# Performance work log

Hardware: AMD Instinct MI355X
Metric: run time of the kernel (lower is better)

Reference implementation:

```python
import jax, jax.numpy as jnp
import numpy as np

DIM = 512
HEADS = 8
RES = 14
HEAD_DIM = DIM // HEADS
N = RES * RES


def _make_bias_idxs(res):
    pts = [(i, j) for i in range(res) for j in range(res)]
    offs = {}
    idxs = []
    for p1 in pts:
        for p2 in pts:
            o = (abs(p1[0] - p2[0]), abs(p1[1] - p2[1]))
            if o not in offs:
                offs[o] = len(offs)
            idxs.append(offs[o])
    return np.asarray(idxs, dtype=np.int32).reshape(res * res, res * res), len(offs)


def setup_inputs() -> dict:
    key = jax.random.key(0)
    ks = jax.random.split(key, 6)
    idxs, n_off = _make_bias_idxs(RES)  # n_off == 196 for res=14
    B = 128
    return {
        "x": jax.random.normal(ks[0], (B, DIM, RES, RES), dtype=jnp.float32),
        "qkv_w": jax.random.normal(ks[1], (3 * DIM, DIM), dtype=jnp.float32) * 0.02,
        "qkv_b": jnp.zeros((3 * DIM,), dtype=jnp.float32),
        "proj_w": jax.random.normal(ks[2], (DIM, DIM), dtype=jnp.float32) * 0.02,
        "proj_b": jnp.zeros((DIM,), dtype=jnp.float32),
        "attention_biases": jax.random.normal(ks[3], (HEADS, n_off), dtype=jnp.float32) * 0.02,
        "bias_idxs": jnp.asarray(idxs),
    }


def reference(x, qkv_w, qkv_b, proj_w, proj_b, attention_biases, bias_idxs):
    B, C, H, W = x.shape
    scale = HEAD_DIM ** -0.5
    # 1x1 conv == channel-wise linear
    qkv = jnp.einsum("oc,bchw->bohw", qkv_w, x) + qkv_b[None, :, None, None]
    q, k, v = jnp.split(qkv, 3, axis=1)
    # [B, heads, head_dim, N]
    q = q.reshape(B, HEADS, HEAD_DIM, N)
    k = k.reshape(B, HEADS, HEAD_DIM, N)
    v = v.reshape(B, HEADS, HEAD_DIM, N)
    attn = jnp.einsum("bhdn,bhdm->bhnm", q, k) * scale  # [B,h,N,N]
    bias = attention_biases[:, bias_idxs]  # gather -> [h,N,N]
    attn = jax.nn.softmax(attn + bias[None], axis=-1)
    out = jnp.einsum("bhnm,bhdm->bhdn", attn, v).reshape(B, C, H, W)
    return jnp.einsum("oc,bchw->bohw", proj_w, out) + proj_b[None, :, None, None]
```

## Files before the change

kernel.cpp:

```cpp
#include <hip/hip_runtime.h>
#include <hip/hip_bf16.h>
#include <math.h>

#define B_     128
#define DIM_   512
#define HEADS_ 8
#define HD_    64
#define N_     196
#define NP_    224
#define NROW_  208
#define SCALE_ 0.125f
#define BSTRIDE (DIM_ * N_)
#define J_     (B_ * NP_)

typedef unsigned short u16;
typedef unsigned int   u32;
typedef __attribute__((ext_vector_type(8))) short bf16x8;
typedef __attribute__((ext_vector_type(4))) float f32x4;

__device__ __forceinline__ u16 f2bf(float f) {
    u32 u = __float_as_uint(f);
    return (u16)((u + 0x7fffu + ((u >> 16) & 1u)) >> 16);
}


__global__ __launch_bounds__(256) void cvt_w2(
    const float* __restrict__ qw, u16* __restrict__ qd,
    const float* __restrict__ pw, u16* __restrict__ pd)
{
    const float* src = blockIdx.y ? pw : qw;
    u16* dst = blockIdx.y ? pd : qd;
    const int nch = blockIdx.y ? (DIM_ * DIM_ / 8) : (3 * DIM_ * DIM_ / 8);
    const int t = blockIdx.x * 256 + threadIdx.x;
    if (t < nch) {
        const int m16 = t & 15, q = (t >> 4) & 3, kb = (t >> 6) & 15, mb = t >> 10;
        const float* s = src + (size_t)(mb * 16 + m16) * DIM_ + kb * 32 + q * 8;
        const float4 v0 = reinterpret_cast<const float4*>(s)[0];
        const float4 v1 = reinterpret_cast<const float4*>(s)[1];
        uint4 o;
        o.x = (u32)f2bf(v0.x) | ((u32)f2bf(v0.y) << 16);
        o.y = (u32)f2bf(v0.z) | ((u32)f2bf(v0.w) << 16);
        o.z = (u32)f2bf(v1.x) | ((u32)f2bf(v1.y) << 16);
        o.w = (u32)f2bf(v1.z) | ((u32)f2bf(v1.w) << 16);
        reinterpret_cast<uint4*>(dst)[t] = o;
    }
}

__global__ __launch_bounds__(256) void cvt_xT(
    const float* __restrict__ x, u16* __restrict__ XT)
{
    __shared__ float tile[64][65];
    const int t = threadIdx.x;
    const int jj = t & 63, ii = t >> 6;
    const int ct = blockIdx.x, ntb = blockIdx.y, b = blockIdx.z;
    const float* xb = x + ((size_t)b * DIM_ + ct * 64) * N_;
    const int n0 = ntb * 64;
    #pragma unroll
    for (int s = 0; s < 16; ++s) {
        const int i = ii + s * 4;
        const int n = n0 + jj;
        tile[i][jj] = (n < N_) ? xb[(size_t)i * N_ + n] : 0.f;
    }
    __syncthreads();
    const int lo = t & 15, hi = t >> 4;
    const int c8 = hi & 7, ng = hi >> 3;
    #pragma unroll
    for (int s = 0; s < 2; ++s) {
        const int n_loc = (s * 2 + ng) * 16 + lo;
        const int nn = n0 + n_loc;
        if (nn < N_) {
            const int j = b * NP_ + nn;
            const int c0 = ct * 64 + c8 * 8;
            u16 vv[8];
            #pragma unroll
            for (int e = 0; e < 8; ++e) vv[e] = f2bf(tile[c8 * 8 + e][n_loc]);
            uint4 o;
            o.x = (u32)vv[0] | ((u32)vv[1] << 16);
            o.y = (u32)vv[2] | ((u32)vv[3] << 16);
            o.z = (u32)vv[4] | ((u32)vv[5] << 16);
            o.w = (u32)vv[6] | ((u32)vv[7] << 16);
            *reinterpret_cast<uint4*>(XT + (size_t)(j >> 4) * 8192
                + (c0 >> 5) * 512 + ((c0 >> 3) & 3) * 128 + (j & 15) * 8) = o;
        }
    }
}

__global__ __launch_bounds__(256) void mk_eb(
    const float* __restrict__ biases, const int* __restrict__ bidx,
    float* __restrict__ EB)
{
    const int n = blockIdx.x, h = blockIdx.y;
    const int m = threadIdx.x;
    if (m < NP_) {
        float v = 0.f;
        if (n < N_ && m < N_) v = __expf(biases[h * N_ + bidx[n * N_ + m]]);
        EB[((size_t)h * NROW_ + n) * NP_ + m] = v;
    }
}

template<bool QKV>
__global__ __launch_bounds__(256) void gemm128(
    const u16* __restrict__ Bt, const u16* __restrict__ W,
    const float* __restrict__ bias,
    u16* __restrict__ o_q, u16* __restrict__ o_k, u16* __restrict__ o_v,
    float* __restrict__ o_f)
{
    const int t = threadIdx.x;
    const int wave = t >> 6, lane = t & 63;
    const int m16 = lane & 15, quad = lane >> 4;

    constexpr int MT  = QKV ? 12 : 4;
    constexpr int NWG = (J_ / 128) * MT;
    const int bid = blockIdx.x;
    const int swz = (bid & 7) * (NWG / 8) + (bid >> 3);
    const int mt = swz % MT;
    const int jt = swz / MT;
    const int m0 = mt * 128, j0 = jt * 128;
    const int wy = wave >> 1, wx = wave & 1;

    const u16* A2 = W  + (size_t)(mt * 8 + wy * 4) * 8192 + quad * 128 + m16 * 8;
    const u16* B2 = Bt + (size_t)(jt * 8 + wx * 4) * 8192 + quad * 128 + m16 * 8;

    f32x4 acc[4][4];
    const f32x4 z4 = {0.f, 0.f, 0.f, 0.f};
    #pragma unroll
    for (int fi = 0; fi < 4; ++fi)
        #pragma unroll
        for (int fj = 0; fj < 4; ++fj) acc[fi][fj] = z4;

    #pragma unroll
    for (int kt = 0; kt < 16; ++kt) {
        bf16x8 af[4], bf[4];
        #pragma unroll
        for (int fi = 0; fi < 4; ++fi)
            af[fi] = *reinterpret_cast<const bf16x8*>(A2 + fi * 8192 + kt * 512);
        #pragma unroll
        for (int fj = 0; fj < 4; ++fj)
            bf[fj] = *reinterpret_cast<const bf16x8*>(B2 + fj * 8192 + kt * 512);
        #pragma unroll
        for (int fi = 0; fi < 4; ++fi)
            #pragma unroll
            for (int fj = 0; fj < 4; ++fj)
                acc[fi][fj] = __builtin_amdgcn_mfma_f32_16x16x32_bf16(af[fi], bf[fj], acc[fi][fj], 0, 0, 0);
    }

    const int mbase = m0 + wy * 64;
    float bb[4][4];
    #pragma unroll
    for (int fi = 0; fi < 4; ++fi)
        #pragma unroll
        for (int r = 0; r < 4; ++r) bb[fi][r] = bias[mbase + fi * 16 + quad * 4 + r];

    if (QKV) {
        const int part = mbase >> 9;
        const int h = (mbase & 511) >> 6;
        #pragma unroll
        for (int fj = 0; fj < 4; ++fj) {
            const int j = j0 + wx * 64 + fj * 16 + m16;
            const u32 b = (u32)j / 224u;
            const int n = j - (int)b * 224;
            if (part < 2) {
                u16* base = (part == 0 ? o_q : o_k) + (((size_t)b * HEADS_ + h) * NP_ + n) * HD_;
                #pragma unroll
                for (int fi = 0; fi < 4; ++fi) {
                    const int d0 = fi * 16 + quad * 4;
                    uint2 pk;
                    pk.x = (u32)f2bf(acc[fi][fj][0] + bb[fi][0]) | ((u32)f2bf(acc[fi][fj][1] + bb[fi][1]) << 16);
                    pk.y = (u32)f2bf(acc[fi][fj][2] + bb[fi][2]) | ((u32)f2bf(acc[fi][fj][3] + bb[fi][3]) << 16);
                    *reinterpret_cast<uint2*>(base + d0) = pk;
                }
            } else {
                u16* vb = o_v + (((size_t)b * HEADS_ + h) * HD_) * NP_ + n;
                #pragma unroll
                for (int fi = 0; fi < 4; ++fi) {
                    const int d0 = fi * 16 + quad * 4;
                    #pragma unroll
                    for (int r = 0; r < 4; ++r)
                        vb[(size_t)(d0 + r) * NP_] = f2bf(acc[fi][fj][r] + bb[fi][r]);
                }
            }
        }
    } else {
        #pragma unroll
        for (int fj = 0; fj < 4; ++fj) {
            const int j = j0 + wx * 64 + fj * 16 + m16;
            const u32 b = (u32)j / 224u;
            const int n = j - (int)b * 224;
            if (n < N_) {
                float* ob = o_f + (size_t)b * BSTRIDE + n;
                #pragma unroll
                for (int fi = 0; fi < 4; ++fi) {
                    const int r0 = mbase + fi * 16 + quad * 4;
                    #pragma unroll
                    for (int r = 0; r < 4; ++r)
                        ob[(size_t)(r0 + r) * N_] = acc[fi][fj][r] + bb[fi][r];
                }
            }
        }
    }
}

__global__ __launch_bounds__(512) void attn_mfma(
    const u16* __restrict__ qT, const u16* __restrict__ kT,
    const u16* __restrict__ vS, const float* __restrict__ EB,
    u16* __restrict__ OT)
{
    __shared__ u16 Ks[224 * 64];
    __shared__ u16 Vs[64 * 232];
    __shared__ u16 P[8][16 * 232];
    const int t = threadIdx.x;
    const int wave = t >> 6, lane = t & 63;
    const int m16 = lane & 15, quad = lane >> 4;
    const int b = blockIdx.x, h = blockIdx.y;
    const u16* qTb = qT + ((size_t)b * HEADS_ + h) * (NP_ * HD_);
    const u16* kTb = kT + ((size_t)b * HEADS_ + h) * (NP_ * HD_);
    const u16* vb  = vS + ((size_t)b * HEADS_ + h) * (HD_ * NP_);
    const float* ebh = EB + (size_t)h * NROW_ * NP_;
    u16* Pw = P[wave];
    const f32x4 z4 = {0.f, 0.f, 0.f, 0.f};

    #pragma unroll
    for (int i = 0; i < 4; ++i) {
        const int c = t + i * 512;
        if (c < 1792) {
            const int row = c >> 3, ch = c & 7;
            const bf16x8 d = *reinterpret_cast<const bf16x8*>(kTb + row * HD_ + ch * 8);
            *reinterpret_cast<bf16x8*>(Ks + row * 64 + ((ch ^ (row & 7)) * 8)) = d;
        }
    }
    #pragma unroll
    for (int i = 0; i < 4; ++i) {
        const int c = t + i * 512;
        if (c < 1792) {
            const u32 row = (u32)c / 28u;
            const int ch = c - (int)row * 28;
            const bf16x8 d = *reinterpret_cast<const bf16x8*>(vb + (size_t)row * NP_ + ch * 8);
            *reinterpret_cast<bf16x8*>(Vs + row * 232 + ch * 8) = d;
        }
    }
    __syncthreads();

    for (int nt = wave; nt < 13; nt += 8) {
        f32x4 s[14];
        #pragma unroll
        for (int mt = 0; mt < 14; ++mt) s[mt] = z4;
        #pragma unroll
        for (int ks = 0; ks < 2; ++ks) {
            const bf16x8 a = *reinterpret_cast<const bf16x8*>(
                qTb + (size_t)(nt * 16 + m16) * HD_ + ks * 32 + quad * 8);
            const int ch = ((ks * 4 + quad) ^ (m16 & 7)) * 8;
            #pragma unroll
            for (int mtile = 0; mtile < 14; ++mtile) {
                const bf16x8 bf = *reinterpret_cast<const bf16x8*>(
                    Ks + (mtile * 16 + m16) * 64 + ch);
                s[mtile] = __builtin_amdgcn_mfma_f32_16x16x32_bf16(a, bf, s[mtile], 0, 0, 0);
            }
        }
        float mx[4] = {-INFINITY, -INFINITY, -INFINITY, -INFINITY};
        #pragma unroll
        for (int mt = 0; mt < 14; ++mt)
            #pragma unroll
            for (int r = 0; r < 4; ++r) mx[r] = fmaxf(mx[r], s[mt][r]);
        #pragma unroll
        for (int off = 1; off < 16; off <<= 1)
            #pragma unroll
            for (int r = 0; r < 4; ++r) mx[r] = fmaxf(mx[r], __shfl_xor(mx[r], off, 64));
        #pragma unroll
        for (int r = 0; r < 4; ++r) mx[r] *= SCALE_;

        const float* ebn = ebh + (size_t)(nt * 16 + quad * 4) * NP_ + m16;
        float sum[4] = {0.f, 0.f, 0.f, 0.f};
        #pragma unroll
        for (int mt = 0; mt < 14; ++mt) {
            #pragma unroll
            for (int r = 0; r < 4; ++r) {
                const float e = __expf(fmaf(s[mt][r], SCALE_, -mx[r])) * ebn[(size_t)r * NP_ + mt * 16];
                s[mt][r] = e;
                sum[r] += e;
            }
        }
        #pragma unroll
        for (int off = 1; off < 16; off <<= 1)
            #pragma unroll
            for (int r = 0; r < 4; ++r) sum[r] += __shfl_xor(sum[r], off, 64);
        float inv[4];
        #pragma unroll
        for (int r = 0; r < 4; ++r) inv[r] = 1.f / sum[r];

        #pragma unroll
        for (int mt = 0; mt < 14; ++mt)
            #pragma unroll
            for (int r = 0; r < 4; ++r)
                Pw[(quad * 4 + r) * 232 + mt * 16 + m16] = f2bf(s[mt][r] * inv[r]);

        f32x4 o[4];
        #pragma unroll
        for (int dt = 0; dt < 4; ++dt) o[dt] = z4;
        #pragma unroll
        for (int ks = 0; ks < 7; ++ks) {
            const bf16x8 a = *reinterpret_cast<const bf16x8*>(Pw + m16 * 232 + ks * 32 + quad * 8);
            #pragma unroll
            for (int dt = 0; dt < 4; ++dt) {
                const bf16x8 bf = *reinterpret_cast<const bf16x8*>(
                    Vs + (dt * 16 + m16) * 232 + ks * 32 + quad * 8);
                o[dt] = __builtin_amdgcn_mfma_f32_16x16x32_bf16(a, bf, o[dt], 0, 0, 0);
            }
        }
        #pragma unroll
        for (int r = 0; r < 4; ++r) {
            const int n = nt * 16 + quad * 4 + r;
            if (n < N_) {
                const int j = b * NP_ + n;
                #pragma unroll
                for (int dt = 0; dt < 4; ++dt) {
                    const int c = h * HD_ + dt * 16 + m16;
                    OT[(size_t)(j >> 4) * 8192 + (c >> 5) * 512
                       + ((c >> 3) & 3) * 128 + (j & 15) * 8 + (c & 7)] = f2bf(o[dt][r]);
                }
            }
        }
    }
}

extern "C" void kernel_launch(void* const* d_in, const int* in_sizes, int n_in,
                              void* d_out, int out_size, void* d_ws, size_t ws_size,
                              hipStream_t stream) {
    const float* x      = (const float*)d_in[0];
    const float* qkv_w  = (const float*)d_in[1];
    const float* qkv_b  = (const float*)d_in[2];
    const float* proj_w = (const float*)d_in[3];
    const float* proj_b = (const float*)d_in[4];
    const float* biases = (const float*)d_in[5];
    const int*   bidx   = (const int*)d_in[6];
    float* out = (float*)d_out;

    char* w = (char*)d_ws;
    u16* XT  = (u16*)w; w += (size_t)B_ * NP_ * DIM_ * 2;
    u16* qTw = (u16*)w; w += (size_t)B_ * HEADS_ * NP_ * HD_ * 2;
    u16* vSw = (u16*)w; w += (size_t)B_ * HEADS_ * HD_ * NP_ * 2;
    float* EB = (float*)w; w += (size_t)HEADS_ * NROW_ * NP_ * 4;
    u16* wq  = (u16*)w; w += (size_t)3 * DIM_ * DIM_ * 2;
    u16* wpj = (u16*)w;
    u16* kTw = (u16*)d_out;

    cvt_w2<<<dim3(384, 2), 256, 0, stream>>>(qkv_w, wq, proj_w, wpj);
    cvt_xT<<<dim3(8, 4, B_), 256, 0, stream>>>(x, XT);
    mk_eb<<<dim3(NROW_, HEADS_), 256, 0, stream>>>(biases, bidx, EB);
    gemm128<true><<<dim3((J_ / 128) * 12), 256, 0, stream>>>(XT, wq, qkv_b, qTw, kTw, vSw, nullptr);
    attn_mfma<<<dim3(B_, HEADS_), 512, 0, stream>>>(qTw, kTw, vSw, EB, XT);
    gemm128<false><<<dim3((J_ / 128) * 4), 256, 0, stream>>>(XT, wpj, proj_b, nullptr, nullptr, nullptr, out);
}
```

Measured before the change: 292.2 us.

## Stage activation tile in LDS and loop over all weight tiles per block

Replaces the per-(m,j) tile GEMM grid with one block per 128-column activation tile. The 128x512 bf16 activation slab is staged into LDS once via global_load_lds, and 8 waves loop over all M tiles, each wave computing a 128x64 output with 8x4 MFMA fragments. This reuses the activation across every weight tile without re-reading it from global memory. In exchange there are fewer blocks (224), a 128KB LDS footprint, more accumulator registers per wave, and weights still read directly from global memory.

```diff
diff --git a/kernel.cpp b/kernel.cpp
--- a/kernel.cpp
+++ b/kernel.cpp
@@ -98,102 +98,117 @@
     }
 }
 
-template<bool QKV>
-__global__ __launch_bounds__(256) void gemm128(
+template<int MT>
+__global__ __launch_bounds__(512) void gemmJ(
     const u16* __restrict__ Bt, const u16* __restrict__ W,
     const float* __restrict__ bias,
     u16* __restrict__ o_q, u16* __restrict__ o_k, u16* __restrict__ o_v,
     float* __restrict__ o_f)
 {
+    __shared__ u16 Bs[8 * 8192];
     const int t = threadIdx.x;
     const int wave = t >> 6, lane = t & 63;
     const int m16 = lane & 15, quad = lane >> 4;
-
-    constexpr int MT  = QKV ? 12 : 4;
-    constexpr int NWG = (J_ / 128) * MT;
-    const int bid = blockIdx.x;
-    const int swz = (bid & 7) * (NWG / 8) + (bid >> 3);
-    const int mt = swz % MT;
-    const int jt = swz / MT;
-    const int m0 = mt * 128, j0 = jt * 128;
-    const int wy = wave >> 1, wx = wave & 1;
-
-    const u16* A2 = W  + (size_t)(mt * 8 + wy * 4) * 8192 + quad * 128 + m16 * 8;
-    const u16* B2 = Bt + (size_t)(jt * 8 + wx * 4) * 8192 + quad * 128 + m16 * 8;
-
-    f32x4 acc[4][4];
+    const int jt = blockIdx.x;
+    const int wx = wave & 1, mtp = wave >> 1;
+    const int j0 = jt * 128;
+
+    {
+        const u16* src = Bt + (size_t)jt * 65536;
+        #pragma unroll
+        for (int i = 0; i < 16; ++i) {
+            const int c = i * 512 + t;
+            __builtin_amdgcn_global_load_lds(
+                (const __attribute__((address_space(1))) void*)(src + c * 8),
+                (__attribute__((address_space(3))) void*)(Bs + c * 8), 16, 0, 0);
+        }
+    }
+    __syncthreads();
+
+    const u16* Wb = W + quad * 128 + m16 * 8;
+    const u16* Bw = Bs + (size_t)(wx * 4) * 8192 + quad * 128 + m16 * 8;
     const f32x4 z4 = {0.f, 0.f, 0.f, 0.f};
-    #pragma unroll
-    for (int fi = 0; fi < 4; ++fi)
-        #pragma unroll
-        for (int fj = 0; fj < 4; ++fj) acc[fi][fj] = z4;
-
-    #pragma unroll
-    for (int kt = 0; kt < 16; ++kt) {
-        bf16x8 af[4], bf[4];
-        #pragma unroll
-        for (int fi = 0; fi < 4; ++fi)
-            af[fi] = *reinterpret_cast<const bf16x8*>(A2 + fi * 8192 + kt * 512);
-        #pragma unroll
-        for (int fj = 0; fj < 4; ++fj)
-            bf[fj] = *reinterpret_cast<const bf16x8*>(B2 + fj * 8192 + kt * 512);
-        #pragma unroll
-        for (int fi = 0; fi < 4; ++fi)
+
+    for (int mi = 0; mi < MT / 4; ++mi) {
+        const int mt = mi * 4 + mtp;
+
+        f32x4 acc[8][4];
+        #pragma unroll
+        for (int fi = 0; fi < 8; ++fi)
+            #pragma unroll
+            for (int fj = 0; fj < 4; ++fj) acc[fi][fj] = z4;
+
+        const u16* Am = Wb + (size_t)(mt * 8) * 8192;
+        #pragma unroll
+        for (int kt = 0; kt < 16; ++kt) {
+            bf16x8 af[8], bf[4];
+            #pragma unroll
+            for (int fi = 0; fi < 8; ++fi)
+                af[fi] = *reinterpret_cast<const bf16x8*>(Am + (size_t)fi * 8192 + kt * 512);
             #pragma unroll
             for (int fj = 0; fj < 4; ++fj)
-                acc[fi][fj] = __builtin_amdgcn_mfma_f32_16x16x32_bf16(af[fi], bf[fj], acc[fi][fj], 0, 0, 0);
-    }
-
-    const int mbase = m0 + wy * 64;
-    float bb[4][4];
-    #pragma unroll
-    for (int fi = 0; fi < 4; ++fi)
-        #pragma unroll
-        for (int r = 0; r < 4; ++r) bb[fi][r] = bias[mbase + fi * 16 + quad * 4 + r];
-
-    if (QKV) {
-        const int part = mbase >> 9;
-        const int h = (mbase & 511) >> 6;
-        #pragma unroll
-        for (int fj = 0; fj < 4; ++fj) {
-            const int j = j0 + wx * 64 + fj * 16 + m16;
-            const u32 b = (u32)j / 224u;
-            const int n = j - (int)b * 224;
-            if (part < 2) {
-                u16* base = (part == 0 ? o_q : o_k) + (((size_t)b * HEADS_ + h) * NP_ + n) * HD_;
-                #pragma unroll
-                for (int fi = 0; fi < 4; ++fi) {
-                    const int d0 = fi * 16 + quad * 4;
-                    uint2 pk;
-                    pk.x = (u32)f2bf(acc[fi][fj][0] + bb[fi][0]) | ((u32)f2bf(acc[fi][fj][1] + bb[fi][1]) << 16);
-                    pk.y = (u32)f2bf(acc[fi][fj][2] + bb[fi][2]) | ((u32)f2bf(acc[fi][fj][3] + bb[fi][3]) << 16);
-                    *reinterpret_cast<uint2*>(base + d0) = pk;
+                bf[fj] = *reinterpret_cast<const bf16x8*>(Bw + (size_t)fj * 8192 + kt * 512);
+            #pragma unroll
+            for (int fi = 0; fi < 8; ++fi)
+                #pragma unroll
+                for (int fj = 0; fj < 4; ++fj)
+                    acc[fi][fj] = __builtin_amdgcn_mfma_f32_16x16x32_bf16(af[fi], bf[fj], acc[fi][fj], 0, 0, 0);
+        }
+
+        #pragma unroll
+        for (int g = 0; g < 2; ++g) {
+            const int mbase = mt * 128 + g * 64;
+            float bb[4][4];
+            #pragma unroll
+            for (int fi = 0; fi < 4; ++fi)
+                #pragma unroll
+                for (int r = 0; r < 4; ++r) bb[fi][r] = bias[mbase + fi * 16 + quad * 4 + r];
+
+            if (MT == 12) {
+                const int part = mbase >> 9;
+                const int h = (mbase & 511) >> 6;
+                #pragma unroll
+                for (int fj = 0; fj < 4; ++fj) {
+                    const int j = j0 + wx * 64 + fj * 16 + m16;
+                    const u32 b = (u32)j / 224u;
+                    const int n = j - (int)b * 224;
+                    if (part < 2) {
+                        u16* base = (part == 0 ? o_q : o_k) + (((size_t)b * HEADS_ + h) * NP_ + n) * HD_;
+                        #pragma unroll
+                        for (int fi = 0; fi < 4; ++fi) {
+                            const int d0 = fi * 16 + quad * 4;
+                            uint2 pk;
+                            pk.x = (u32)f2bf(acc[g * 4 + fi][fj][0] + bb[fi][0]) | ((u32)f2bf(acc[g * 4 + fi][fj][1] + bb[fi][1]) << 16);
+                            pk.y = (u32)f2bf(acc[g * 4 + fi][fj][2] + bb[fi][2]) | ((u32)f2bf(acc[g * 4 + fi][fj][3] + bb[fi][3]) << 16);
+                            *reinterpret_cast<uint2*>(base + d0) = pk;
+                        }
+                    } else {
+                        u16* vb = o_v + (((size_t)b * HEADS_ + h) * HD_) * NP_ + n;
+                        #pragma unroll
+                        for (int fi = 0; fi < 4; ++fi) {
+                            const int d0 = fi * 16 + quad * 4;
+                            #pragma unroll
+                            for (int r = 0; r < 4; ++r)
+                                vb[(size_t)(d0 + r) * NP_] = f2bf(acc[g * 4 + fi][fj][r] + bb[fi][r]);
+                        }
+                    }
                 }
             } else {
-                u16* vb = o_v + (((size_t)b * HEADS_ + h) * HD_) * NP_ + n;
-                #pragma unroll
-                for (int fi = 0; fi < 4; ++fi) {
-                    const int d0 = fi * 16 + quad * 4;
-                    #pragma unroll
-                    for (int r = 0; r < 4; ++r)
-                        vb[(size_t)(d0 + r) * NP_] = f2bf(acc[fi][fj][r] + bb[fi][r]);
-                }
-            }
-        }
-    } else {
-        #pragma unroll
-        for (int fj = 0; fj < 4; ++fj) {
-            const int j = j0 + wx * 64 + fj * 16 + m16;
-            const u32 b = (u32)j / 224u;
-            const int n = j - (int)b * 224;
-            if (n < N_) {
-                float* ob = o_f + (size_t)b * BSTRIDE + n;
-                #pragma unroll
-                for (int fi = 0; fi < 4; ++fi) {
-                    const int r0 = mbase + fi * 16 + quad * 4;
-                    #pragma unroll
-                    for (int r = 0; r < 4; ++r)
-                        ob[(size_t)(r0 + r) * N_] = acc[fi][fj][r] + bb[fi][r];
+                #pragma unroll
+                for (int fj = 0; fj < 4; ++fj) {
+                    const int j = j0 + wx * 64 + fj * 16 + m16;
+                    const u32 b = (u32)j / 224u;
+                    const int n = j - (int)b * 224;
+                    if (n < N_) {
+                        float* ob = o_f + (size_t)b * BSTRIDE + n;
+                        #pragma unroll
+                        for (int fi = 0; fi < 4; ++fi) {
+                            const int r0 = mbase + fi * 16 + quad * 4;
+                            #pragma unroll
+                            for (int r = 0; r < 4; ++r)
+                                ob[(size_t)(r0 + r) * N_] = acc[g * 4 + fi][fj][r] + bb[fi][r];
+                        }
+                    }
                 }
             }
         }
@@ -346,7 +361,7 @@
     cvt_w2<<<dim3(384, 2), 256, 0, stream>>>(qkv_w, wq, proj_w, wpj);
     cvt_xT<<<dim3(8, 4, B_), 256, 0, stream>>>(x, XT);
     mk_eb<<<dim3(NROW_, HEADS_), 256, 0, stream>>>(biases, bidx, EB);
-    gemm128<true><<<dim3((J_ / 128) * 12), 256, 0, stream>>>(XT, wq, qkv_b, qTw, kTw, vSw, nullptr);
+    gemmJ<12><<<dim3(J_ / 128), 512, 0, stream>>>(XT, wq, qkv_b, qTw, kTw, vSw, nullptr);
     attn_mfma<<<dim3(B_, HEADS_), 512, 0, stream>>>(qTw, kTw, vSw, EB, XT);
-    gemm128<false><<<dim3((J_ / 128) * 4), 256, 0, stream>>>(XT, wpj, proj_b, nullptr, nullptr, nullptr, out);
-}
+    gemmJ<4><<<dim3(J_ / 128), 512, 0, stream>>>(XT, wpj, proj_b, nullptr, nullptr, nullptr, out);
+}
```

Result: slower. 340.3 us (+16.5%).

## Stage GEMM tiles through double-buffered LDS and merge prep kernels

Applied to the files above, without the earlier changes.

Folds the three preprocessing kernels (weight conversion, x transpose, exp-bias table) into one launch that dispatches on block index. The GEMM now loads its A and B tiles with global_load_lds into double-buffered shared memory, prefetching the next k-chunk while MFMAs run on the current one. Before, each wave read fragments straight from global memory. The intent is less launch overhead, better reuse of tiles across waves, and overlap of memory traffic with compute. In exchange the GEMM uses 64KB of LDS per block, which lowers occupancy, and adds a barrier per k-step.

```diff
diff --git a/kernel.cpp b/kernel.cpp
--- a/kernel.cpp
+++ b/kernel.cpp
@@ -22,89 +22,96 @@
     u32 u = __float_as_uint(f);
     return (u16)((u + 0x7fffu + ((u >> 16) & 1u)) >> 16);
 }
-
-
-__global__ __launch_bounds__(256) void cvt_w2(
+__device__ __forceinline__ void gload_lds16(const u16* g, u16* l) {
+    __builtin_amdgcn_global_load_lds(
+        (const __attribute__((address_space(1))) void*)g,
+        (__attribute__((address_space(3))) void*)l, 16, 0, 0);
+}
+
+
+__global__ __launch_bounds__(256) void prep(
+    const float* __restrict__ x, u16* __restrict__ XT,
     const float* __restrict__ qw, u16* __restrict__ qd,
-    const float* __restrict__ pw, u16* __restrict__ pd)
-{
-    const float* src = blockIdx.y ? pw : qw;
-    u16* dst = blockIdx.y ? pd : qd;
-    const int nch = blockIdx.y ? (DIM_ * DIM_ / 8) : (3 * DIM_ * DIM_ / 8);
-    const int t = blockIdx.x * 256 + threadIdx.x;
-    if (t < nch) {
-        const int m16 = t & 15, q = (t >> 4) & 3, kb = (t >> 6) & 15, mb = t >> 10;
-        const float* s = src + (size_t)(mb * 16 + m16) * DIM_ + kb * 32 + q * 8;
-        const float4 v0 = reinterpret_cast<const float4*>(s)[0];
-        const float4 v1 = reinterpret_cast<const float4*>(s)[1];
-        uint4 o;
-        o.x = (u32)f2bf(v0.x) | ((u32)f2bf(v0.y) << 16);
-        o.y = (u32)f2bf(v0.z) | ((u32)f2bf(v0.w) << 16);
-        o.z = (u32)f2bf(v1.x) | ((u32)f2bf(v1.y) << 16);
-        o.w = (u32)f2bf(v1.z) | ((u32)f2bf(v1.w) << 16);
-        reinterpret_cast<uint4*>(dst)[t] = o;
-    }
-}
-
-__global__ __launch_bounds__(256) void cvt_xT(
-    const float* __restrict__ x, u16* __restrict__ XT)
-{
-    __shared__ float tile[64][65];
-    const int t = threadIdx.x;
-    const int jj = t & 63, ii = t >> 6;
-    const int ct = blockIdx.x, ntb = blockIdx.y, b = blockIdx.z;
-    const float* xb = x + ((size_t)b * DIM_ + ct * 64) * N_;
-    const int n0 = ntb * 64;
-    #pragma unroll
-    for (int s = 0; s < 16; ++s) {
-        const int i = ii + s * 4;
-        const int n = n0 + jj;
-        tile[i][jj] = (n < N_) ? xb[(size_t)i * N_ + n] : 0.f;
-    }
-    __syncthreads();
-    const int lo = t & 15, hi = t >> 4;
-    const int c8 = hi & 7, ng = hi >> 3;
-    #pragma unroll
-    for (int s = 0; s < 2; ++s) {
-        const int n_loc = (s * 2 + ng) * 16 + lo;
-        const int nn = n0 + n_loc;
-        if (nn < N_) {
-            const int j = b * NP_ + nn;
-            const int c0 = ct * 64 + c8 * 8;
-            u16 vv[8];
-            #pragma unroll
-            for (int e = 0; e < 8; ++e) vv[e] = f2bf(tile[c8 * 8 + e][n_loc]);
-            uint4 o;
-            o.x = (u32)vv[0] | ((u32)vv[1] << 16);
-            o.y = (u32)vv[2] | ((u32)vv[3] << 16);
-            o.z = (u32)vv[4] | ((u32)vv[5] << 16);
-            o.w = (u32)vv[6] | ((u32)vv[7] << 16);
-            *reinterpret_cast<uint4*>(XT + (size_t)(j >> 4) * 8192
-                + (c0 >> 5) * 512 + ((c0 >> 3) & 3) * 128 + (j & 15) * 8) = o;
-        }
-    }
-}
-
-__global__ __launch_bounds__(256) void mk_eb(
+    const float* __restrict__ pw, u16* __restrict__ pd,
     const float* __restrict__ biases, const int* __restrict__ bidx,
     float* __restrict__ EB)
 {
-    const int n = blockIdx.x, h = blockIdx.y;
-    const int m = threadIdx.x;
-    if (m < NP_) {
-        float v = 0.f;
-        if (n < N_ && m < N_) v = __expf(biases[h * N_ + bidx[n * N_ + m]]);
-        EB[((size_t)h * NROW_ + n) * NP_ + m] = v;
+    const int id = blockIdx.x;
+    const int t = threadIdx.x;
+    if (id < 4096) {
+        __shared__ float tile[64][65];
+        const int jj = t & 63, ii = t >> 6;
+        const int ct = id & 7, ntb = (id >> 3) & 3, b = id >> 5;
+        const float* xb = x + ((size_t)b * DIM_ + ct * 64) * N_;
+        const int n0 = ntb * 64;
+        #pragma unroll
+        for (int s = 0; s < 16; ++s) {
+            const int i = ii + s * 4;
+            const int n = n0 + jj;
+            tile[i][jj] = (n < N_) ? xb[(size_t)i * N_ + n] : 0.f;
+        }
+        __syncthreads();
+        const int lo = t & 15, hi = t >> 4;
+        const int c8 = hi & 7, ng = hi >> 3;
+        #pragma unroll
+        for (int s = 0; s < 2; ++s) {
+            const int n_loc = (s * 2 + ng) * 16 + lo;
+            const int nn = n0 + n_loc;
+            if (nn < N_) {
+                const int j = b * NP_ + nn;
+                const int c0 = ct * 64 + c8 * 8;
+                u16 vv[8];
+                #pragma unroll
+                for (int e = 0; e < 8; ++e) vv[e] = f2bf(tile[c8 * 8 + e][n_loc]);
+                uint4 o;
+                o.x = (u32)vv[0] | ((u32)vv[1] << 16);
+                o.y = (u32)vv[2] | ((u32)vv[3] << 16);
+                o.z = (u32)vv[4] | ((u32)vv[5] << 16);
+                o.w = (u32)vv[6] | ((u32)vv[7] << 16);
+                *reinterpret_cast<uint4*>(XT + (size_t)(j >> 4) * 8192
+                    + (c0 >> 5) * 512 + ((c0 >> 3) & 3) * 128 + (j & 15) * 8) = o;
+            }
+        }
+    } else if (id < 5760) {
+        const int e = id - 4096;
+        const int n = e % NROW_, h = e / NROW_;
+        const int m = t;
+        if (m < NP_) {
+            float v = 0.f;
+            if (n < N_ && m < N_) v = __expf(biases[h * N_ + bidx[n * N_ + m]]);
+            EB[((size_t)h * NROW_ + n) * NP_ + m] = v;
+        }
+    } else {
+        const bool pj = id >= 6144;
+        const int cb = id - (pj ? 6144 : 5760);
+        const float* src = pj ? pw : qw;
+        u16* dst = pj ? pd : qd;
+        const int nch = pj ? (DIM_ * DIM_ / 8) : (3 * DIM_ * DIM_ / 8);
+        const int c = cb * 256 + t;
+        if (c < nch) {
+            const int m16 = c & 15, q = (c >> 4) & 3, kb = (c >> 6) & 15, mb = c >> 10;
+            const float* s = src + (size_t)(mb * 16 + m16) * DIM_ + kb * 32 + q * 8;
+            const float4 v0 = reinterpret_cast<const float4*>(s)[0];
+            const float4 v1 = reinterpret_cast<const float4*>(s)[1];
+            uint4 o;
+            o.x = (u32)f2bf(v0.x) | ((u32)f2bf(v0.y) << 16);
+            o.y = (u32)f2bf(v0.z) | ((u32)f2bf(v0.w) << 16);
+            o.z = (u32)f2bf(v1.x) | ((u32)f2bf(v1.y) << 16);
+            o.w = (u32)f2bf(v1.z) | ((u32)f2bf(v1.w) << 16);
+            reinterpret_cast<uint4*>(dst)[c] = o;
+        }
     }
 }
 
 template<bool QKV>
-__global__ __launch_bounds__(256) void gemm128(
+__global__ __launch_bounds__(256) void gemmF(
     const u16* __restrict__ Bt, const u16* __restrict__ W,
     const float* __restrict__ bias,
     u16* __restrict__ o_q, u16* __restrict__ o_k, u16* __restrict__ o_v,
     float* __restrict__ o_f)
 {
+    __shared__ u16 As[2][8192];
+    __shared__ u16 Bs[2][8192];
     const int t = threadIdx.x;
     const int wave = t >> 6, lane = t & 63;
     const int m16 = lane & 15, quad = lane >> 4;
@@ -118,8 +125,10 @@
     const int m0 = mt * 128, j0 = jt * 128;
     const int wy = wave >> 1, wx = wave & 1;
 
-    const u16* A2 = W  + (size_t)(mt * 8 + wy * 4) * 8192 + quad * 128 + m16 * 8;
-    const u16* B2 = Bt + (size_t)(jt * 8 + wx * 4) * 8192 + quad * 128 + m16 * 8;
+    const u16* gAb = W  + (size_t)(mt * 8) * 8192;
+    const u16* gBb = Bt + (size_t)(jt * 8) * 8192;
+
+    const int roff = quad * 128 + m16 * 8;
 
     f32x4 acc[4][4];
     const f32x4 z4 = {0.f, 0.f, 0.f, 0.f};
@@ -129,19 +138,39 @@
         for (int fj = 0; fj < 4; ++fj) acc[fi][fj] = z4;
 
     #pragma unroll
-    for (int kt = 0; kt < 16; ++kt) {
-        bf16x8 af[4], bf[4];
-        #pragma unroll
-        for (int fi = 0; fi < 4; ++fi)
-            af[fi] = *reinterpret_cast<const bf16x8*>(A2 + fi * 8192 + kt * 512);
-        #pragma unroll
-        for (int fj = 0; fj < 4; ++fj)
-            bf[fj] = *reinterpret_cast<const bf16x8*>(B2 + fj * 8192 + kt * 512);
-        #pragma unroll
-        for (int fi = 0; fi < 4; ++fi)
+    for (int c = 0; c < 4; ++c) {
+        const int g = c * 256 + t;
+        const int f = g >> 7, s = (g >> 6) & 1, ch = g & 63;
+        gload_lds16(gAb + (size_t)f * 8192 + s * 512 + ch * 8, As[0] + g * 8);
+        gload_lds16(gBb + (size_t)f * 8192 + s * 512 + ch * 8, Bs[0] + g * 8);
+    }
+    for (int kt = 0; kt < 8; ++kt) {
+        const int cur = kt & 1;
+        __syncthreads();
+        if (kt < 7) {
+            #pragma unroll
+            for (int c = 0; c < 4; ++c) {
+                const int g = c * 256 + t;
+                const int f = g >> 7, s = (g >> 6) & 1, ch = g & 63;
+                gload_lds16(gAb + (size_t)f * 8192 + ((kt + 1) * 2 + s) * 512 + ch * 8, As[cur ^ 1] + g * 8);
+                gload_lds16(gBb + (size_t)f * 8192 + ((kt + 1) * 2 + s) * 512 + ch * 8, Bs[cur ^ 1] + g * 8);
+            }
+        }
+        #pragma unroll
+        for (int ks = 0; ks < 2; ++ks) {
+            bf16x8 af[4], bf[4];
+            #pragma unroll
+            for (int fi = 0; fi < 4; ++fi)
+                af[fi] = *reinterpret_cast<const bf16x8*>(As[cur] + ((wy * 4 + fi) * 2 + ks) * 512 + roff);
             #pragma unroll
             for (int fj = 0; fj < 4; ++fj)
-                acc[fi][fj] = __builtin_amdgcn_mfma_f32_16x16x32_bf16(af[fi], bf[fj], acc[fi][fj], 0, 0, 0);
+                bf[fj] = *reinterpret_cast<const bf16x8*>(Bs[cur] + ((wx * 4 + fj) * 2 + ks) * 512 + roff);
+            #pragma unroll
+            for (int fi = 0; fi < 4; ++fi)
+                #pragma unroll
+                for (int fj = 0; fj < 4; ++fj)
+                    acc[fi][fj] = __builtin_amdgcn_mfma_f32_16x16x32_bf16(af[fi], bf[fj], acc[fi][fj], 0, 0, 0);
+        }
     }
 
     const int mbase = m0 + wy * 64;
@@ -343,10 +372,8 @@
     u16* wpj = (u16*)w;
     u16* kTw = (u16*)d_out;
 
-    cvt_w2<<<dim3(384, 2), 256, 0, stream>>>(qkv_w, wq, proj_w, wpj);
-    cvt_xT<<<dim3(8, 4, B_), 256, 0, stream>>>(x, XT);
-    mk_eb<<<dim3(NROW_, HEADS_), 256, 0, stream>>>(biases, bidx, EB);
-    gemm128<true><<<dim3((J_ / 128) * 12), 256, 0, stream>>>(XT, wq, qkv_b, qTw, kTw, vSw, nullptr);
+    prep<<<dim3(6272), 256, 0, stream>>>(x, XT, qkv_w, wq, proj_w, wpj, biases, bidx, EB);
+    gemmF<true><<<dim3((J_ / 128) * 12), 256, 0, stream>>>(XT, wq, qkv_b, qTw, kTw, vSw, nullptr);
     attn_mfma<<<dim3(B_, HEADS_), 512, 0, stream>>>(qTw, kTw, vSw, EB, XT);
-    gemm128<false><<<dim3((J_ / 128) * 4), 256, 0, stream>>>(XT, wpj, proj_b, nullptr, nullptr, nullptr, out);
-}
+    gemmF<false><<<dim3((J_ / 128) * 4), 256, 0, stream>>>(XT, wpj, proj_b, nullptr, nullptr, nullptr, out);
+}
```

Result: faster. 261.8 us (-10.4%).
